# Optimization experiments

Hardware: AMD Instinct MI355X
Metric: run time of the kernel (lower is better)

Reference implementation:

```python
import jax, jax.numpy as jnp
import numpy as np

N, E, D, ED = 50000, 500000, 128, 10
EPS = 1e-5


def _glorot(key, shape):
    return jax.random.normal(key, shape, jnp.float32) / np.sqrt(shape[0]).astype(np.float32)


def setup_inputs() -> dict:
    key = jax.random.key(0)
    ks = jax.random.split(key, 8)
    x = jax.random.normal(ks[0], (N, D), jnp.float32)
    edge_index = jax.random.randint(ks[1], (2, E), 0, N, jnp.int32)
    edge_attr = jax.random.normal(ks[2], (E, ED), jnp.float32)
    # edge encoder: Linear(edge_dim -> F_in)
    W_ee = _glorot(ks[3], (ED, D)); b_ee = jnp.zeros((D,), jnp.float32)
    # pre MLP (pre_layers=1): Linear(3*F_in -> F_in) on cat([x_i, x_j, e])
    W_pre = _glorot(ks[4], (3 * D, D)); b_pre = jnp.zeros((D,), jnp.float32)
    # post MLP (post_layers=1): Linear((4 aggr * 3 scalers + 1)*F_in -> F_out)
    W_post = _glorot(ks[5], (13 * D, D)); b_post = jnp.zeros((D,), jnp.float32)
    # final lin: Linear(towers*F_out -> out_channels)
    W_lin = _glorot(ks[6], (D, D)); b_lin = jnp.zeros((D,), jnp.float32)
    return {"x": x, "edge_attr": edge_attr, "W_ee": W_ee, "b_ee": b_ee,
            "W_pre": W_pre, "b_pre": b_pre, "W_post": W_post, "b_post": b_post,
            "W_lin": W_lin, "b_lin": b_lin, "edge_index": edge_index}


def reference(x, edge_attr, W_ee, b_ee, W_pre, b_pre, W_post, b_post, W_lin, b_lin, edge_index):
    n = x.shape[0]
    src, dst = edge_index[0], edge_index[1]  # x_j = x[src], x_i = x[dst]

    # --- message: pre-MLP over cat([x_i, x_j, edge_enc]) ---
    ea = edge_attr @ W_ee + b_ee                                   # [E, D]
    h = jnp.concatenate([x[dst], x[src], ea], axis=-1)             # [E, 3D]
    m = h @ W_pre + b_pre                                          # [E, D]

    # --- multi-aggregation at target nodes: mean / max / min / std ---
    cnt = jax.ops.segment_sum(jnp.ones((m.shape[0],), x.dtype), dst, num_segments=n)  # [N]
    deg = jnp.maximum(cnt, 1.0)[:, None]                           # clamp(1), [N,1]
    has_edge = (cnt > 0)[:, None]
    mean = jax.ops.segment_sum(m, dst, num_segments=n) / deg
    mean_sq = jax.ops.segment_sum(m * m, dst, num_segments=n) / deg
    std = jnp.sqrt(jax.nn.relu(mean_sq - mean * mean) + EPS)
    mx = jnp.where(has_edge, jax.ops.segment_max(m, dst, num_segments=n), 0.0)
    mn = jnp.where(has_edge, jax.ops.segment_min(m, dst, num_segments=n), 0.0)
    agg = jnp.concatenate([mean, mx, mn, std], axis=-1)            # [N, 4D]

    # --- degree scalers: identity / amplification / attenuation ---
    avg_log = jnp.mean(jnp.log(cnt + 1.0))                         # avg_deg['log']
    s_log = jnp.log(deg + 1.0)                                     # [N,1]
    scaled = jnp.concatenate([agg, agg * (s_log / avg_log), agg * (avg_log / s_log)], axis=-1)  # [N,12D]

    # --- post MLP on cat([x, aggregated]) then final linear ---
    out = jnp.concatenate([x, scaled], axis=-1) @ W_post + b_post  # [N, D]
    return out @ W_lin + b_lin
```

## Files before the change

kernel.cpp:

```cpp
#include <hip/hip_runtime.h>
#include <hip/hip_bf16.h>
#include <float.h>
#include <math.h>

#define N_NODES 50000
#define N_EDGES 500000
#define D 128
#define ED 10
#define EPS_PNA 1e-5f
#define SCAN_NTILES 49

typedef __hip_bfloat16 bf16;
typedef unsigned short ushort;
typedef unsigned int uint;
typedef __attribute__((ext_vector_type(8))) short short8;
typedef __attribute__((ext_vector_type(4))) float f32x4;

__device__ __forceinline__ ushort f2bf(float f) {
    __hip_bfloat16 h = __float2bfloat16(f);
    return *reinterpret_cast<ushort*>(&h);
}
__device__ __forceinline__ float bf2f(ushort u) {
    return __uint_as_float(((uint)u) << 16);
}

__global__ void k_hist(const int* __restrict__ ei, int* __restrict__ cnt) {
    int e = blockIdx.x * blockDim.x + threadIdx.x;
    if (e < N_EDGES) atomicAdd(&cnt[ei[N_EDGES + e]], 1);
}

__global__ __launch_bounds__(256) void k_scanA(const int* __restrict__ cnt,
                                               int* __restrict__ bsum,
                                               float* __restrict__ blog) {
    const int t = threadIdx.x;
    const int base = blockIdx.x * 1024;
    int s = 0; float ls = 0.f;
    #pragma unroll
    for (int k = 0; k < 4; ++k) {
        const int idx = base + t + k * 256;
        if (idx < N_NODES) {
            const int c = cnt[idx];
            s += c;
            ls += logf((float)c + 1.0f);
        }
    }
    #pragma unroll
    for (int off = 32; off > 0; off >>= 1) {
        s += __shfl_down(s, off, 64);
        ls += __shfl_down(ls, off, 64);
    }
    __shared__ int ws[4]; __shared__ float wl[4];
    const int wv = t >> 6, l = t & 63;
    if (l == 0) { ws[wv] = s; wl[wv] = ls; }
    __syncthreads();
    if (t == 0) {
        bsum[blockIdx.x] = ws[0] + ws[1] + ws[2] + ws[3];
        blog[blockIdx.x] = wl[0] + wl[1] + wl[2] + wl[3];
    }
}

__global__ void k_scanB(const int* __restrict__ bsum, const float* __restrict__ blog,
                        int* __restrict__ boff, int* __restrict__ rowstart,
                        float* __restrict__ avglog) {
    const int t = threadIdx.x;
    const int v = (t < SCAN_NTILES) ? bsum[t] : 0;
    const float lg = (t < SCAN_NTILES) ? blog[t] : 0.f;
    int s = v;
    #pragma unroll
    for (int off = 1; off < 64; off <<= 1) {
        const int u = __shfl_up(s, off, 64);
        if (t >= off) s += u;
    }
    if (t < SCAN_NTILES) boff[t] = s - v;
    if (t == 63) rowstart[N_NODES] = s;
    float lt = lg;
    #pragma unroll
    for (int off = 32; off > 0; off >>= 1) lt += __shfl_down(lt, off, 64);
    if (t == 0) avglog[0] = lt * (1.0f / (float)N_NODES);
}

__global__ __launch_bounds__(256) void k_scanC(const int* __restrict__ cnt,
                                               const int* __restrict__ boff,
                                               int* __restrict__ rowstart,
                                               int* __restrict__ cursor) {
    const int t = threadIdx.x, lane = t & 63, wv = t >> 6;
    const int base = blockIdx.x * 1024;
    int c[4]; int ts = 0;
    #pragma unroll
    for (int k = 0; k < 4; ++k) {
        const int idx = base + t * 4 + k;
        c[k] = (idx < N_NODES) ? cnt[idx] : 0;
        ts += c[k];
    }
    int s = ts;
    #pragma unroll
    for (int off = 1; off < 64; off <<= 1) {
        const int u = __shfl_up(s, off, 64);
        if (lane >= off) s += u;
    }
    __shared__ int wtot[4], woff[4];
    if (lane == 63) wtot[wv] = s;
    __syncthreads();
    if (t == 0) {
        int r = 0;
        #pragma unroll
        for (int i = 0; i < 4; ++i) { woff[i] = r; r += wtot[i]; }
    }
    __syncthreads();
    int excl = boff[blockIdx.x] + woff[wv] + (s - ts);
    #pragma unroll
    for (int k = 0; k < 4; ++k) {
        const int idx = base + t * 4 + k;
        if (idx < N_NODES) { rowstart[idx] = excl; cursor[idx] = excl; }
        excl += c[k];
    }
}

__global__ void k_scatter(const int* __restrict__ ei, int* __restrict__ cursor,
                          int2* __restrict__ csr_se) {
    int e = blockIdx.x * blockDim.x + threadIdx.x;
    if (e < N_EDGES) {
        const int dst = ei[N_EDGES + e];
        const int pos = atomicAdd(&cursor[dst], 1);
        csr_se[pos] = make_int2(ei[e], e);
    }
}

__global__ __launch_bounds__(256) void k_wprep(
    const float* __restrict__ Wee, const float* __restrict__ bee,
    const float* __restrict__ Wpre, const float* __restrict__ bpre,
    const float* __restrict__ Wpost, const float* __restrict__ bpost,
    const float* __restrict__ Wlin, const float* __restrict__ blin,
    float* __restrict__ W4, float* __restrict__ bp,
    ushort* __restrict__ WxT,
    ushort* __restrict__ WaT,
    float* __restrict__ b_comb,
    int* __restrict__ cnt)
{
    __shared__ float smem[128 * 128];
    const int t = threadIdx.x;
    const int bx = blockIdx.x;

    if (bx < 104) {
        float* Wl = smem;
        for (int i = t; i < 128 * 128 / 4; i += 256)
            ((float4*)Wl)[i] = ((const float4*)Wlin)[i];
        __syncthreads();
        const int j = t & 127, rp = t >> 7;
        const int kr0 = bx * 16 + rp * 8;
        for (int r = 0; r < 8; ++r) {
            const int kr = kr0 + r;
            const float* wrow = Wpost + (size_t)kr * 128;
            float acc = 0.f;
            #pragma unroll 8
            for (int m = 0; m < 128; ++m) acc += wrow[m] * Wl[m * 128 + j];
            const ushort v = f2bf(acc);
            if (kr < 128)       WxT[(256 + j) * 128 + kr] = v;
            else if (kr < 640)  WaT[(size_t)j * 512 + (kr - 128)] = v;
            else if (kr < 1152) WaT[(size_t)(128 + j) * 512 + (kr - 640)] = v;
            else                WaT[(size_t)(256 + j) * 512 + (kr - 1152)] = v;
        }
        if (bx == 0 && t < 128) {
            float acc = 0.f;
            #pragma unroll 8
            for (int m = 0; m < 128; ++m) acc += bpost[m] * Wl[m * 128 + t];
            b_comb[t] = acc + blin[t];
        }
    } else if (bx == 104) {
        float* wee_s = smem;
        float* bee_s = smem + ED * D;
        for (int i = t; i < ED * D; i += 256) wee_s[i] = Wee[i];
        if (t < 128) bee_s[t] = bee[t];
        __syncthreads();
        if (t < 128) {
            float acc[ED];
            #pragma unroll
            for (int r = 0; r < ED; ++r) acc[r] = 0.f;
            float bacc = 0.f;
            for (int k = 0; k < D; ++k) {
                const float w3 = Wpre[(size_t)(2 * D + k) * D + t];
                #pragma unroll
                for (int r = 0; r < ED; ++r) acc[r] += wee_s[r * D + k] * w3;
                bacc += bee_s[k] * w3;
            }
            #pragma unroll
            for (int r = 0; r < ED; ++r) W4[r * D + t] = acc[r];
            bp[t] = bpre[t] + bacc;
        }
    } else if (bx < 121) {
        const int slice = (bx < 113) ? 0 : 1;
        const int id = (bx - (slice ? 113 : 105)) * 256 + t;
        const float* src = Wpre + (size_t)slice * 128 * 128;
        ushort* dst = WxT + (size_t)slice * 128 * 128;
        const int col = id & 127;
        const int k0 = (id >> 7) * 8;
        ushort tmp[8];
        #pragma unroll
        for (int r = 0; r < 8; ++r) tmp[r] = f2bf(src[(size_t)(k0 + r) * 128 + col]);
        *(uint4*)(dst + (size_t)col * 128 + k0) = *(uint4*)tmp;
    } else {
        const int i = (bx - 121) * 256 + t;
        if (i < N_NODES) cnt[i] = 0;
    }
}

__global__ __launch_bounds__(256) void k_xgemm(
    const float* __restrict__ x, const ushort* __restrict__ WxT,
    const float* __restrict__ b_comb,
    ushort* __restrict__ Y1b, ushort* __restrict__ Y2b, ushort* __restrict__ Y0b)
{
    __shared__ __align__(16) ushort Alds[128 * 136];
    __shared__ __align__(16) ushort Hlds[128 * 136];
    const int t = threadIdx.x;
    const int nb = blockIdx.x * 128;

    #pragma unroll
    for (int g = 0; g < 8; ++g) {
        const int idx = t + g * 256;
        const int row = idx >> 4, kk = (idx & 15) * 8;
        const int node = nb + row;
        uint4 v = make_uint4(0u, 0u, 0u, 0u);
        if (node < N_NODES) {
            const float4 f0 = *(const float4*)(x + (size_t)node * 128 + kk);
            const float4 f1 = *(const float4*)(x + (size_t)node * 128 + kk + 4);
            __hip_bfloat162 p0 = __float22bfloat162_rn(make_float2(f0.x, f0.y));
            __hip_bfloat162 p1 = __float22bfloat162_rn(make_float2(f0.z, f0.w));
            __hip_bfloat162 p2 = __float22bfloat162_rn(make_float2(f1.x, f1.y));
            __hip_bfloat162 p3 = __float22bfloat162_rn(make_float2(f1.z, f1.w));
            v.x = *(uint*)&p0; v.y = *(uint*)&p1; v.z = *(uint*)&p2; v.w = *(uint*)&p3;
        }
        *(uint4*)&Hlds[row * 136 + kk] = v;
    }

    const int w = t >> 6, l = t & 63;
    const int wr = w >> 1, wc = w & 1;
    const int quad = l >> 4, lr = l & 15;

    for (int sy = 0; sy < 3; ++sy) {
        __syncthreads();
        #pragma unroll
        for (int g = 0; g < 8; ++g) {
            const int idx = t + g * 256;
            const int row = idx >> 4, kk = (idx & 15) * 8;
            *(uint4*)&Alds[row * 136 + kk] =
                *(const uint4*)(WxT + ((size_t)sy * 128 + row) * 128 + kk);
        }
        __syncthreads();

        f32x4 acc[4][4];
        #pragma unroll
        for (int i = 0; i < 4; ++i)
            #pragma unroll
            for (int j = 0; j < 4; ++j) acc[i][j] = (f32x4){0.f, 0.f, 0.f, 0.f};

        #pragma unroll
        for (int s = 0; s < 4; ++s) {
            short8 av[4], bv[4];
            #pragma unroll
            for (int i = 0; i < 4; ++i)
                av[i] = *(const short8*)&Alds[(wr * 64 + i * 16 + lr) * 136 + s * 32 + quad * 8];
            #pragma unroll
            for (int j = 0; j < 4; ++j)
                bv[j] = *(const short8*)&Hlds[(wc * 64 + j * 16 + lr) * 136 + s * 32 + quad * 8];
            #pragma unroll
            for (int i = 0; i < 4; ++i)
                #pragma unroll
                for (int j = 0; j < 4; ++j)
                    acc[i][j] = __builtin_amdgcn_mfma_f32_16x16x32_bf16(av[i], bv[j], acc[i][j], 0, 0, 0);
        }

        ushort* dst = (sy == 0) ? Y1b : (sy == 1) ? Y2b : Y0b;
        #pragma unroll
        for (int i = 0; i < 4; ++i) {
            const int col = wr * 64 + i * 16 + quad * 4;
            float b0 = 0.f, b1 = 0.f, b2 = 0.f, b3 = 0.f;
            if (sy == 2) {
                b0 = b_comb[col]; b1 = b_comb[col + 1];
                b2 = b_comb[col + 2]; b3 = b_comb[col + 3];
            }
            #pragma unroll
            for (int j = 0; j < 4; ++j) {
                const int node = nb + wc * 64 + j * 16 + lr;
                if (node < N_NODES) {
                    const f32x4 v = acc[i][j];
                    ushort pk[4];
                    pk[0] = f2bf(v.x + b0); pk[1] = f2bf(v.y + b1);
                    pk[2] = f2bf(v.z + b2); pk[3] = f2bf(v.w + b3);
                    *(uint2*)(dst + (size_t)node * 128 + col) = *(uint2*)pk;
                }
            }
        }
    }
}

__global__ __launch_bounds__(256) void k_pull(
    const float* __restrict__ eattr, const float* __restrict__ W4,
    const float* __restrict__ bp, const ushort* __restrict__ Y1b,
    const ushort* __restrict__ Y2b,
    const int* __restrict__ rowstart,
    const int2* __restrict__ csr_se,
    ushort* __restrict__ aggB)
{
    __shared__ float2 w4s[ED][64];
    const int t = threadIdx.x;
    for (int i = t; i < ED * 64; i += 256)
        w4s[i >> 6][i & 63] = ((const float2*)W4)[i];
    __syncthreads();

    const int wv = t >> 6, l = t & 63;
    const int n = blockIdx.x * 4 + wv;
    const int r0 = rowstart[n], r1 = rowstart[n + 1];
    const int d = r1 - r0;

    float s0 = 0.f, s1 = 0.f, ss0 = 0.f, ss1 = 0.f;
    float mx0 = -FLT_MAX, mx1 = -FLT_MAX, mn0 = FLT_MAX, mn1 = FLT_MAX;
    const __hip_bfloat162* Y2p = (const __hip_bfloat162*)Y2b;

    int2 se = (d > 0) ? csr_se[r0] : make_int2(0, 0);
    for (int i = r0; i < r1; ++i) {
        const int2 cur = se;
        const int inext = (i + 1 < r1) ? (i + 1) : i;
        se = csr_se[inext];
        const float2 y2 = __bfloat1622float2(Y2p[(size_t)cur.x * 64 + l]);
        const float2* ea2 = (const float2*)(eattr + (size_t)cur.y * ED);
        float q0 = 0.f, q1 = 0.f;
        #pragma unroll
        for (int r = 0; r < 5; ++r) {
            const float2 a = ea2[r];
            const float2 wA = w4s[2 * r][l];
            const float2 wB = w4s[2 * r + 1][l];
            q0 += a.x * wA.x + a.y * wB.x;
            q1 += a.x * wA.y + a.y * wB.y;
        }
        const float z0 = y2.x + q0, z1 = y2.y + q1;
        s0 += z0; s1 += z1;
        ss0 += z0 * z0; ss1 += z1 * z1;
        mx0 = fmaxf(mx0, z0); mx1 = fmaxf(mx1, z1);
        mn0 = fminf(mn0, z0); mn1 = fminf(mn1, z1);
    }

    const float2 bpw = ((const float2*)bp)[l];
    const float2 y1 = __bfloat1622float2(((const __hip_bfloat162*)Y1b)[(size_t)n * 64 + l]);
    float mean0, mean1, vmx0, vmx1, vmn0, vmn1, st0, st1;
    if (d > 0) {
        const float inv = 1.f / (float)d;
        const float mz0 = s0 * inv, mz1 = s1 * inv;
        const float c0 = y1.x + bpw.x, c1 = y1.y + bpw.y;
        mean0 = mz0 + c0; mean1 = mz1 + c1;
        st0 = sqrtf(fmaxf(ss0 * inv - mz0 * mz0, 0.f) + EPS_PNA);
        st1 = sqrtf(fmaxf(ss1 * inv - mz1 * mz1, 0.f) + EPS_PNA);
        vmx0 = mx0 + c0; vmx1 = mx1 + c1;
        vmn0 = mn0 + c0; vmn1 = mn1 + c1;
    } else {
        mean0 = mean1 = 0.f;
        vmx0 = vmx1 = vmn0 = vmn1 = 0.f;
        st0 = st1 = sqrtf(EPS_PNA);
    }
    __hip_bfloat162* aggv = (__hip_bfloat162*)aggB;
    const size_t b0 = (size_t)n * 256;
    aggv[b0 + l]       = __float22bfloat162_rn(make_float2(mean0, mean1));
    aggv[b0 + 64 + l]  = __float22bfloat162_rn(make_float2(vmx0, vmx1));
    aggv[b0 + 128 + l] = __float22bfloat162_rn(make_float2(vmn0, vmn1));
    aggv[b0 + 192 + l] = __float22bfloat162_rn(make_float2(st0, st1));
}

__global__ __launch_bounds__(256) void k_agg(
    const ushort* __restrict__ aggB,
    const ushort* __restrict__ WaT,
    const ushort* __restrict__ Y0b,
    const int* __restrict__ cnt, const float* __restrict__ avglog,
    float* __restrict__ out)
{
    __shared__ __align__(16) ushort Alds[128 * 72];
    __shared__ __align__(16) ushort Hlds[64 * 72];
    __shared__ float r1s[64], r2s[64];

    const int t = threadIdx.x;
    const int nb = blockIdx.x * 64;
    if (t < 64) {
        const int node = nb + t;
        float deg = 1.f;
        if (node < N_NODES) deg = fmaxf((float)cnt[node], 1.f);
        const float sl = logf(deg + 1.f);
        const float al = avglog[0];
        r1s[t] = sl / al;
        r2s[t] = al / sl;
    }

    const int w = t >> 6, l = t & 63;
    const int wr = w >> 1, wc = w & 1;
    const int quad = l >> 4, lr = l & 15;

    f32x4 comb[4][2];
    #pragma unroll
    for (int i = 0; i < 4; ++i)
        #pragma unroll
        for (int j = 0; j < 2; ++j) comb[i][j] = (f32x4){0.f, 0.f, 0.f, 0.f};

    #define STAGE_A(SL)                                                           \
        _Pragma("unroll")                                                         \
        for (int g = 0; g < 4; ++g) {                                             \
            const int idx = t + g * 256;                                          \
            const int row = idx >> 3, kk = (idx & 7) * 8;                         \
            *(uint4*)&Alds[row * 72 + kk] =                                       \
                *(const uint4*)(WaT + ((size_t)((SL) * 128 + row)) * 512 + k0 + kk); \
        }

    #define MFMA_EPOCH(SL)                                                        \
        {                                                                         \
            f32x4 acc[4][2];                                                      \
            _Pragma("unroll")                                                     \
            for (int i = 0; i < 4; ++i)                                           \
                _Pragma("unroll")                                                 \
                for (int j = 0; j < 2; ++j) acc[i][j] = (f32x4){0.f,0.f,0.f,0.f}; \
            _Pragma("unroll")                                                     \
            for (int s = 0; s < 2; ++s) {                                         \
                short8 av[4], bv[2];                                              \
                _Pragma("unroll")                                                 \
                for (int i = 0; i < 4; ++i)                                       \
                    av[i] = *(const short8*)&Alds[(wr*64 + i*16 + lr)*72 + s*32 + quad*8]; \
                _Pragma("unroll")                                                 \
                for (int j = 0; j < 2; ++j)                                       \
                    bv[j] = *(const short8*)&Hlds[(wc*32 + j*16 + lr)*72 + s*32 + quad*8]; \
                _Pragma("unroll")                                                 \
                for (int i = 0; i < 4; ++i)                                       \
                    _Pragma("unroll")                                             \
                    for (int j = 0; j < 2; ++j)                                   \
                        acc[i][j] = __builtin_amdgcn_mfma_f32_16x16x32_bf16(av[i], bv[j], acc[i][j], 0, 0, 0); \
            }                                                                     \
            _Pragma("unroll")                                                     \
            for (int j = 0; j < 2; ++j) {                                         \
                const int nl = wc * 32 + j * 16 + lr;                             \
                const float r = ((SL) == 0) ? 1.f : ((SL) == 1) ? r1s[nl] : r2s[nl]; \
                _Pragma("unroll")                                                 \
                for (int i = 0; i < 4; ++i) {                                     \
                    comb[i][j].x += r * acc[i][j].x;                              \
                    comb[i][j].y += r * acc[i][j].y;                              \
                    comb[i][j].z += r * acc[i][j].z;                              \
                    comb[i][j].w += r * acc[i][j].w;                              \
                }                                                                 \
            }                                                                     \
        }

    for (int kc = 0; kc < 8; ++kc) {
        const int k0 = kc * 64;
        __syncthreads();
        #pragma unroll
        for (int g = 0; g < 2; ++g) {
            const int idx = t + g * 256;
            const int row = idx >> 3, kk = (idx & 7) * 8;
            const int node = nb + row;
            uint4 v = make_uint4(0u, 0u, 0u, 0u);
            if (node < N_NODES)
                v = *(const uint4*)(aggB + (size_t)node * 512 + k0 + kk);
            *(uint4*)&Hlds[row * 72 + kk] = v;
        }
        STAGE_A(0);
        __syncthreads();
        MFMA_EPOCH(0);
        __syncthreads();
        STAGE_A(1);
        __syncthreads();
        MFMA_EPOCH(1);
        __syncthreads();
        STAGE_A(2);
        __syncthreads();
        MFMA_EPOCH(2);
    }
    #undef STAGE_A
    #undef MFMA_EPOCH

    #pragma unroll
    for (int i = 0; i < 4; ++i) {
        const int col = wr * 64 + i * 16 + quad * 4;
        #pragma unroll
        for (int j = 0; j < 2; ++j) {
            const int node = nb + wc * 32 + j * 16 + lr;
            if (node < N_NODES) {
                const uint2 y0 = *(const uint2*)(Y0b + (size_t)node * 128 + col);
                const ushort* yp = (const ushort*)&y0;
                const f32x4 v = comb[i][j];
                *(float4*)(out + (size_t)node * 128 + col) =
                    make_float4(v.x + bf2f(yp[0]), v.y + bf2f(yp[1]),
                                v.z + bf2f(yp[2]), v.w + bf2f(yp[3]));
            }
        }
    }
}

extern "C" void kernel_launch(void* const* d_in, const int* in_sizes, int n_in,
                              void* d_out, int out_size, void* d_ws, size_t ws_size,
                              hipStream_t stream) {
    const float* x     = (const float*)d_in[0];
    const float* eattr = (const float*)d_in[1];
    const float* Wee   = (const float*)d_in[2];
    const float* bee   = (const float*)d_in[3];
    const float* Wpre  = (const float*)d_in[4];
    const float* bpre  = (const float*)d_in[5];
    const float* Wpost = (const float*)d_in[6];
    const float* bpost = (const float*)d_in[7];
    const float* Wlin  = (const float*)d_in[8];
    const float* blin  = (const float*)d_in[9];
    const int*   ei    = (const int*)d_in[10];
    float* out = (float*)d_out;

    ushort* aggB = (ushort*)d_ws;
    ushort* Y1b  = aggB + (size_t)N_NODES * 512;
    ushort* Y2b  = Y1b  + (size_t)N_NODES * 128;
    ushort* Y0b  = Y2b  + (size_t)N_NODES * 128;
    ushort* WxT  = Y0b  + (size_t)N_NODES * 128;
    ushort* WaT  = WxT + 384 * 128;
    float*  W4   = (float*)(WaT + 384 * 512);
    float*  bp   = W4 + ED * D;
    float*  b_comb = bp + D;
    float*  avglog = b_comb + D;
    int*   cnt      = (int*)(avglog + 4);
    int*   rowstart = cnt + N_NODES;
    int*   cursor   = rowstart + N_NODES + 2;
    int2*  csr_se   = (int2*)(cursor + N_NODES + 2);
    int*   bsum     = (int*)(csr_se + N_EDGES);
    float* blog     = (float*)(bsum + 64);
    int*   boff     = (int*)(blog + 64);

    k_wprep<<<317, 256, 0, stream>>>(Wee, bee, Wpre, bpre, Wpost, bpost, Wlin, blin,
                                     W4, bp, WxT, WaT, b_comb, cnt);
    k_hist<<<(N_EDGES + 255) / 256, 256, 0, stream>>>(ei, cnt);
    k_scanA<<<SCAN_NTILES, 256, 0, stream>>>(cnt, bsum, blog);
    k_scanB<<<1, 64, 0, stream>>>(bsum, blog, boff, rowstart, avglog);
    k_scanC<<<SCAN_NTILES, 256, 0, stream>>>(cnt, boff, rowstart, cursor);
    k_scatter<<<(N_EDGES + 255) / 256, 256, 0, stream>>>(ei, cursor, csr_se);
    k_xgemm<<<(N_NODES + 127) / 128, 256, 0, stream>>>(x, WxT, b_comb,
                                                       Y1b, Y2b, Y0b);
    k_pull<<<N_NODES / 4, 256, 0, stream>>>(eattr, W4, bp, Y1b, Y2b,
                                            rowstart, csr_se, aggB);
    k_agg<<<(N_NODES + 63) / 64, 256, 0, stream>>>(aggB, WaT, Y0b, cnt, avglog, out);
}
```

Before: 343.9 us.

## Fuse histogram into node GEMM, pack edge attrs into CSR, write Y0 to output

The degree histogram now runs as extra blocks of the node GEMM kernel, so there is one fewer launch and the atomics overlap with the MFMA work. The scatter kernel copies each edge's 10 attributes plus its source index into a 48-byte CSR record. The pull loop then reads these records contiguously instead of gathering edge_attr by edge id. The Y0 term is written straight to the output in fp32 and read back by the final kernel, which drops the bf16 Y0 buffer and its rounding. In exchange, the scatter writes far more data and the final kernel does an extra fp32 read-modify-write of the output.

```diff
diff --git a/kernel.cpp b/kernel.cpp
--- a/kernel.cpp
+++ b/kernel.cpp
@@ -9,6 +9,8 @@
 #define ED 10
 #define EPS_PNA 1e-5f
 #define SCAN_NTILES 49
+#define XGEMM_BLOCKS 391
+#define HIST_BLOCKS 1954
 
 typedef __hip_bfloat16 bf16;
 typedef unsigned short ushort;
@@ -22,11 +24,6 @@
 }
 __device__ __forceinline__ float bf2f(ushort u) {
     return __uint_as_float(((uint)u) << 16);
-}
-
-__global__ void k_hist(const int* __restrict__ ei, int* __restrict__ cnt) {
-    int e = blockIdx.x * blockDim.x + threadIdx.x;
-    if (e < N_EDGES) atomicAdd(&cnt[ei[N_EDGES + e]], 1);
 }
 
 __global__ __launch_bounds__(256) void k_scanA(const int* __restrict__ cnt,
@@ -116,13 +113,21 @@
     }
 }
 
-__global__ void k_scatter(const int* __restrict__ ei, int* __restrict__ cursor,
-                          int2* __restrict__ csr_se) {
+__global__ void k_scatter(const int* __restrict__ ei, const float* __restrict__ eattr,
+                          int* __restrict__ cursor, uint4* __restrict__ csr_rec) {
     int e = blockIdx.x * blockDim.x + threadIdx.x;
     if (e < N_EDGES) {
         const int dst = ei[N_EDGES + e];
+        const int src = ei[e];
+        const float2* ea2 = (const float2*)(eattr + (size_t)e * ED);
+        const float2 a0 = ea2[0], a1 = ea2[1], a2 = ea2[2], a3 = ea2[3], a4 = ea2[4];
         const int pos = atomicAdd(&cursor[dst], 1);
-        csr_se[pos] = make_int2(ei[e], e);
+        uint4* o = csr_rec + (size_t)pos * 3;
+        o[0] = make_uint4(__float_as_uint(a0.x), __float_as_uint(a0.y),
+                          __float_as_uint(a1.x), __float_as_uint(a1.y));
+        o[1] = make_uint4(__float_as_uint(a2.x), __float_as_uint(a2.y),
+                          __float_as_uint(a3.x), __float_as_uint(a3.y));
+        o[2] = make_uint4(__float_as_uint(a4.x), __float_as_uint(a4.y), (uint)src, 0u);
     }
 }
 
@@ -204,14 +209,21 @@
     }
 }
 
-__global__ __launch_bounds__(256) void k_xgemm(
+__global__ __launch_bounds__(256) void k_hx(
+    const int* __restrict__ ei, int* __restrict__ cnt,
     const float* __restrict__ x, const ushort* __restrict__ WxT,
     const float* __restrict__ b_comb,
-    ushort* __restrict__ Y1b, ushort* __restrict__ Y2b, ushort* __restrict__ Y0b)
+    ushort* __restrict__ Y1b, ushort* __restrict__ Y2b, float* __restrict__ out)
 {
+    const int t = threadIdx.x;
+    if (blockIdx.x >= XGEMM_BLOCKS) {
+        const int e = (blockIdx.x - XGEMM_BLOCKS) * 256 + t;
+        if (e < N_EDGES) atomicAdd(&cnt[ei[N_EDGES + e]], 1);
+        return;
+    }
+
     __shared__ __align__(16) ushort Alds[128 * 136];
     __shared__ __align__(16) ushort Hlds[128 * 136];
-    const int t = threadIdx.x;
     const int nb = blockIdx.x * 128;
 
     #pragma unroll
@@ -269,24 +281,25 @@
                     acc[i][j] = __builtin_amdgcn_mfma_f32_16x16x32_bf16(av[i], bv[j], acc[i][j], 0, 0, 0);
         }
 
-        ushort* dst = (sy == 0) ? Y1b : (sy == 1) ? Y2b : Y0b;
         #pragma unroll
         for (int i = 0; i < 4; ++i) {
             const int col = wr * 64 + i * 16 + quad * 4;
-            float b0 = 0.f, b1 = 0.f, b2 = 0.f, b3 = 0.f;
-            if (sy == 2) {
-                b0 = b_comb[col]; b1 = b_comb[col + 1];
-                b2 = b_comb[col + 2]; b3 = b_comb[col + 3];
-            }
             #pragma unroll
             for (int j = 0; j < 4; ++j) {
                 const int node = nb + wc * 64 + j * 16 + lr;
                 if (node < N_NODES) {
                     const f32x4 v = acc[i][j];
-                    ushort pk[4];
-                    pk[0] = f2bf(v.x + b0); pk[1] = f2bf(v.y + b1);
-                    pk[2] = f2bf(v.z + b2); pk[3] = f2bf(v.w + b3);
-                    *(uint2*)(dst + (size_t)node * 128 + col) = *(uint2*)pk;
+                    if (sy == 2) {
+                        *(float4*)(out + (size_t)node * 128 + col) =
+                            make_float4(v.x + b_comb[col],     v.y + b_comb[col + 1],
+                                        v.z + b_comb[col + 2], v.w + b_comb[col + 3]);
+                    } else {
+                        ushort* dst = (sy == 0) ? Y1b : Y2b;
+                        ushort pk[4];
+                        pk[0] = f2bf(v.x); pk[1] = f2bf(v.y);
+                        pk[2] = f2bf(v.z); pk[3] = f2bf(v.w);
+                        *(uint2*)(dst + (size_t)node * 128 + col) = *(uint2*)pk;
+                    }
                 }
             }
         }
@@ -294,11 +307,10 @@
 }
 
 __global__ __launch_bounds__(256) void k_pull(
-    const float* __restrict__ eattr, const float* __restrict__ W4,
+    const uint4* __restrict__ csr_rec, const float* __restrict__ W4,
     const float* __restrict__ bp, const ushort* __restrict__ Y1b,
     const ushort* __restrict__ Y2b,
     const int* __restrict__ rowstart,
-    const int2* __restrict__ csr_se,
     ushort* __restrict__ aggB)
 {
     __shared__ float2 w4s[ED][64];
@@ -316,27 +328,40 @@
     float mx0 = -FLT_MAX, mx1 = -FLT_MAX, mn0 = FLT_MAX, mn1 = FLT_MAX;
     const __hip_bfloat162* Y2p = (const __hip_bfloat162*)Y2b;
 
-    int2 se = (d > 0) ? csr_se[r0] : make_int2(0, 0);
+    uint4 ra, rb, rc;
+    if (d > 0) {
+        const uint4* rp = csr_rec + (size_t)r0 * 3;
+        ra = rp[0]; rb = rp[1]; rc = rp[2];
+    }
     for (int i = r0; i < r1; ++i) {
-        const int2 cur = se;
         const int inext = (i + 1 < r1) ? (i + 1) : i;
-        se = csr_se[inext];
-        const float2 y2 = __bfloat1622float2(Y2p[(size_t)cur.x * 64 + l]);
-        const float2* ea2 = (const float2*)(eattr + (size_t)cur.y * ED);
+        const uint4* rp = csr_rec + (size_t)inext * 3;
+        const uint4 na = rp[0], nb = rp[1], nc = rp[2];
+
+        const int src = (int)rc.z;
+        const float2 y2 = __bfloat1622float2(Y2p[(size_t)src * 64 + l]);
+
+        float ea[10];
+        ea[0] = __uint_as_float(ra.x); ea[1] = __uint_as_float(ra.y);
+        ea[2] = __uint_as_float(ra.z); ea[3] = __uint_as_float(ra.w);
+        ea[4] = __uint_as_float(rb.x); ea[5] = __uint_as_float(rb.y);
+        ea[6] = __uint_as_float(rb.z); ea[7] = __uint_as_float(rb.w);
+        ea[8] = __uint_as_float(rc.x); ea[9] = __uint_as_float(rc.y);
+
         float q0 = 0.f, q1 = 0.f;
         #pragma unroll
-        for (int r = 0; r < 5; ++r) {
-            const float2 a = ea2[r];
-            const float2 wA = w4s[2 * r][l];
-            const float2 wB = w4s[2 * r + 1][l];
-            q0 += a.x * wA.x + a.y * wB.x;
-            q1 += a.x * wA.y + a.y * wB.y;
+        for (int r = 0; r < ED; ++r) {
+            const float2 wv2 = w4s[r][l];
+            q0 += ea[r] * wv2.x;
+            q1 += ea[r] * wv2.y;
         }
         const float z0 = y2.x + q0, z1 = y2.y + q1;
         s0 += z0; s1 += z1;
         ss0 += z0 * z0; ss1 += z1 * z1;
         mx0 = fmaxf(mx0, z0); mx1 = fmaxf(mx1, z1);
         mn0 = fminf(mn0, z0); mn1 = fminf(mn1, z1);
+
+        ra = na; rb = nb; rc = nc;
     }
 
     const float2 bpw = ((const float2*)bp)[l];
@@ -367,7 +392,6 @@
 __global__ __launch_bounds__(256) void k_agg(
     const ushort* __restrict__ aggB,
     const ushort* __restrict__ WaT,
-    const ushort* __restrict__ Y0b,
     const int* __restrict__ cnt, const float* __restrict__ avglog,
     float* __restrict__ out)
 {
@@ -477,12 +501,11 @@
         for (int j = 0; j < 2; ++j) {
             const int node = nb + wc * 32 + j * 16 + lr;
             if (node < N_NODES) {
-                const uint2 y0 = *(const uint2*)(Y0b + (size_t)node * 128 + col);
-                const ushort* yp = (const ushort*)&y0;
+                float* op = out + (size_t)node * 128 + col;
+                const float4 cur = *(const float4*)op;
                 const f32x4 v = comb[i][j];
-                *(float4*)(out + (size_t)node * 128 + col) =
-                    make_float4(v.x + bf2f(yp[0]), v.y + bf2f(yp[1]),
-                                v.z + bf2f(yp[2]), v.w + bf2f(yp[3]));
+                *(float4*)op = make_float4(cur.x + v.x, cur.y + v.y,
+                                           cur.z + v.z, cur.w + v.w);
             }
         }
     }
@@ -507,8 +530,7 @@
     ushort* aggB = (ushort*)d_ws;
     ushort* Y1b  = aggB + (size_t)N_NODES * 512;
     ushort* Y2b  = Y1b  + (size_t)N_NODES * 128;
-    ushort* Y0b  = Y2b  + (size_t)N_NODES * 128;
-    ushort* WxT  = Y0b  + (size_t)N_NODES * 128;
+    ushort* WxT  = Y2b  + (size_t)N_NODES * 128;
     ushort* WaT  = WxT + 384 * 128;
     float*  W4   = (float*)(WaT + 384 * 512);
     float*  bp   = W4 + ED * D;
@@ -516,22 +538,21 @@
     float*  avglog = b_comb + D;
     int*   cnt      = (int*)(avglog + 4);
     int*   rowstart = cnt + N_NODES;
-    int*   cursor   = rowstart + N_NODES + 2;
-    int2*  csr_se   = (int2*)(cursor + N_NODES + 2);
-    int*   bsum     = (int*)(csr_se + N_EDGES);
+    int*   cursor   = rowstart + N_NODES + 4;
+    uint4* csr_rec  = (uint4*)(cursor + N_NODES);
+    int*   bsum     = (int*)(csr_rec + (size_t)N_EDGES * 3);
     float* blog     = (float*)(bsum + 64);
     int*   boff     = (int*)(blog + 64);
 
     k_wprep<<<317, 256, 0, stream>>>(Wee, bee, Wpre, bpre, Wpost, bpost, Wlin, blin,
                                      W4, bp, WxT, WaT, b_comb, cnt);
-    k_hist<<<(N_EDGES + 255) / 256, 256, 0, stream>>>(ei, cnt);
+    k_hx<<<XGEMM_BLOCKS + HIST_BLOCKS, 256, 0, stream>>>(ei, cnt, x, WxT, b_comb,
+                                                         Y1b, Y2b, out);
     k_scanA<<<SCAN_NTILES, 256, 0, stream>>>(cnt, bsum, blog);
     k_scanB<<<1, 64, 0, stream>>>(bsum, blog, boff, rowstart, avglog);
     k_scanC<<<SCAN_NTILES, 256, 0, stream>>>(cnt, boff, rowstart, cursor);
-    k_scatter<<<(N_EDGES + 255) / 256, 256, 0, stream>>>(ei, cursor, csr_se);
-    k_xgemm<<<(N_NODES + 127) / 128, 256, 0, stream>>>(x, WxT, b_comb,
-                                                       Y1b, Y2b, Y0b);
-    k_pull<<<N_NODES / 4, 256, 0, stream>>>(eattr, W4, bp, Y1b, Y2b,
-                                            rowstart, csr_se, aggB);
-    k_agg<<<(N_NODES + 63) / 64, 256, 0, stream>>>(aggB, WaT, Y0b, cnt, avglog, out);
-}
+    k_scatter<<<(N_EDGES + 255) / 256, 256, 0, stream>>>(ei, eattr, cursor, csr_rec);
+    k_pull<<<N_NODES / 4, 256, 0, stream>>>(csr_rec, W4, bp, Y1b, Y2b,
+                                            rowstart, aggB);
+    k_agg<<<(N_NODES + 63) / 64, 256, 0, stream>>>(aggB, WaT, cnt, avglog, out);
+}
```

New measurement: 315.6 us. 1.09x faster.
